# Kernel optimization log

Measured on AMD Instinct MI355X. Metric: run time of the kernel, lower is better.

The kernel has to match this reference:

```python
import jax, jax.numpy as jnp
import numpy as np

N = 10000   # num_nodes
P = 32      # input_dim
Q = 64      # output_dim
K = 2       # diffusion_steps
B = 32      # batch
E = 160000  # edges per transition matrix (avg degree 16)
M = 2 * K + 1  # num_matrices (dual random walk)


def setup_inputs() -> dict:
    key = jax.random.key(0)
    ks = jax.random.split(key, 8)
    inputs = jax.random.normal(ks[0], (B, N * P), dtype=jnp.float32)
    trans1_idx = jax.random.randint(ks[1], (2, E), 0, N, dtype=jnp.int32)
    trans1_val = jax.random.uniform(ks[2], (E,), dtype=jnp.float32)
    trans2_idx = jax.random.randint(ks[3], (2, E), 0, N, dtype=jnp.int32)
    trans2_val = jax.random.uniform(ks[4], (E,), dtype=jnp.float32)
    weight = jax.random.normal(ks[5], (P * M, Q), dtype=jnp.float32) * (1.414 / np.sqrt(P * M))
    bias = jnp.zeros((Q,), dtype=jnp.float32)
    return {"inputs": inputs, "trans1_idx": trans1_idx, "trans1_val": trans1_val,
            "trans2_idx": trans2_idx, "trans2_val": trans2_val,
            "weight": weight, "bias": bias}


def _spmm(idx, val, x):
    # sparse [N,N] (COO rows=idx[0], cols=idx[1]) @ dense x [N, F]
    gathered = val[:, None] * x[idx[1]]            # [E, F]
    return jax.ops.segment_sum(gathered, idx[0], num_segments=N)


def reference(inputs, trans1_idx, trans1_val, trans2_idx, trans2_val, weight, bias):
    batch_size = inputs.shape[0]
    # [B, N*P] -> [N, P*B] (matches torch transpose/reshape sequence)
    x0_base = inputs.reshape(batch_size, N, P).transpose(1, 2, 0).reshape(N, P * batch_size)
    xs = [x0_base]
    for idx, val in ((trans1_idx, trans1_val), (trans2_idx, trans2_val)):
        x0 = x0_base
        x1 = _spmm(idx, val, x0)
        xs.append(x1)
        for _ in range(2, K + 1):
            x2 = 2.0 * _spmm(idx, val, x1) - x0
            xs.append(x2)
            x1, x0 = x2, x1
    x = jnp.stack(xs)                                   # [M, N, P*B]
    x = x.reshape(M, N, P, batch_size).transpose(3, 1, 2, 0)  # [B, N, P, M]
    x = x.reshape(batch_size * N, P * M)
    out = x @ weight + bias                             # [B*N, Q]
    return out.reshape(batch_size, N * Q)
```

## Files before the change

kernel.cpp:

```cpp
#include <hip/hip_runtime.h>
#include <hip/hip_bf16.h>

#define NN 10000
#define PP 32
#define QQ 64
#define EE 160000
#define FF 1024
#define NQ 640000
#define SLOTS 64

typedef __attribute__((ext_vector_type(8))) short sh8;
typedef __attribute__((ext_vector_type(8))) __bf16 bf8v;
typedef __attribute__((ext_vector_type(4))) float f32x4;

__device__ __forceinline__ short f2bf(float f) {
    return __builtin_bit_cast(short, __float2bfloat16(f));
}

__global__ __launch_bounds__(256)
void pre_kernel(const float* __restrict__ in, short* __restrict__ x0,
                const float* __restrict__ W, short* __restrict__ wt,
                int* __restrict__ cnt, int2* __restrict__ ed1, int2* __restrict__ ed2) {
    int t = threadIdx.x;
    if (blockIdx.x == 0) {
#pragma unroll
        for (int j = 0; j < 40; ++j) {
            int idx = t + j * 256;
            int k = idx >> 6, q = idx & 63;
            int p = k / 5;
            int m = k - p * 5;
            wt[q * 160 + m * 32 + p] = f2bf(W[idx]);
        }
        return;
    }
    int n = blockIdx.x - 1;
    int b = t >> 3;
    int p0 = (t & 7) * 4;
    float4 v = *(const float4*)(in + (size_t)b * (NN * PP) + (size_t)n * PP + p0);
    short4 s = make_short4(f2bf(v.x), f2bf(v.y), f2bf(v.z), f2bf(v.w));
    *(short4*)(x0 + (size_t)n * FF + b * 32 + p0) = s;
    if (t < 32)      *(int4*)(ed1 + n * SLOTS + t * 2) = make_int4(0, 0, 0, 0);
    else if (t < 64) *(int4*)(ed2 + n * SLOTS + (t - 32) * 2) = make_int4(0, 0, 0, 0);
    else if (t == 64) { cnt[n] = 0; cnt[NN + n] = 0; }
}

__global__ __launch_bounds__(256)
void scatter_kernel(const int* __restrict__ t1i, const float* __restrict__ t1v,
                    const int* __restrict__ t2i, const float* __restrict__ t2v,
                    int* __restrict__ cnt, int2* __restrict__ ed1, int2* __restrict__ ed2) {
    int e = blockIdx.x * 256 + threadIdx.x;
    const int* idx; const float* val; int* cn; int2* ed; int ee;
    if (e < EE) { idx = t1i; val = t1v; cn = cnt;      ed = ed1; ee = e; }
    else        { idx = t2i; val = t2v; cn = cnt + NN; ed = ed2; ee = e - EE; }
    int r = idx[ee];
    int c = idx[EE + ee];
    int pos = atomicAdd(&cn[r], 1);
    if (pos < SLOTS) ed[r * SLOTS + pos] = make_int2(c, __float_as_int(val[ee]));
}

__global__ __launch_bounds__(256)
void spmm_kernel(const int* __restrict__ cnt, const int2* __restrict__ ed1,
                 const int2* __restrict__ ed2,
                 const short* __restrict__ x1s, const short* __restrict__ x2s,
                 short* __restrict__ out1, short* __restrict__ out2,
                 const short* __restrict__ sub, float alpha) {
    int bid = blockIdx.x;
    int c = bid & 7;
    int rest = bid >> 3;
    int rb = rest % 625;
    int g = rest / 625;
    int fbase = c * 128;
    int wid  = threadIdx.x >> 6;
    int lane = threadIdx.x & 63;
    int grp  = lane >> 4;
    int l8   = (lane & 15) * 8;
    int n = rb * 16 + wid * 4 + grp;

    const int2* ed; const __bf16* x; short* out; int cn;
    if (g == 0) { ed = ed1 + n * SLOTS; x = (const __bf16*)x1s; out = out1; cn = cnt[n]; }
    else        { ed = ed2 + n * SLOTS; x = (const __bf16*)x2s; out = out2; cn = cnt[NN + n]; }
    cn = min(cn, SLOTS);
    int iters = (cn + 3) >> 2;
    const __bf16* xp = x + fbase + l8;

    float acc[8];
#pragma unroll
    for (int j = 0; j < 8; ++j) acc[j] = 0.f;

    for (int it = 0; it < iters; ++it) {
        int4 dA = *(const int4*)(ed);
        int4 dB = *(const int4*)(ed + 2);
        ed += 4;
        bf8v xa = *(const bf8v*)(xp + ((size_t)(unsigned)dA.x << 10));
        bf8v xb = *(const bf8v*)(xp + ((size_t)(unsigned)dA.z << 10));
        bf8v xc = *(const bf8v*)(xp + ((size_t)(unsigned)dB.x << 10));
        bf8v xd = *(const bf8v*)(xp + ((size_t)(unsigned)dB.z << 10));
        float v0 = __int_as_float(dA.y), v1 = __int_as_float(dA.w);
        float v2 = __int_as_float(dB.y), v3 = __int_as_float(dB.w);
#pragma unroll
        for (int j = 0; j < 8; ++j) {
            acc[j] = fmaf((float)xa[j], v0, acc[j]);
            acc[j] = fmaf((float)xb[j], v1, acc[j]);
            acc[j] = fmaf((float)xc[j], v2, acc[j]);
            acc[j] = fmaf((float)xd[j], v3, acc[j]);
        }
    }

    size_t obase = (size_t)n * FF + fbase + l8;
    sh8 o;
    if (sub) {
        bf8v s = *(const bf8v*)((const __bf16*)sub + obase);
#pragma unroll
        for (int j = 0; j < 8; ++j) o[j] = f2bf(alpha * acc[j] - (float)s[j]);
    } else {
#pragma unroll
        for (int j = 0; j < 8; ++j) o[j] = f2bf(acc[j]);
    }
    *(sh8*)(out + obase) = o;
}

__global__ __launch_bounds__(256)
void gemm_mfma_kernel(const short* __restrict__ xs, const short* __restrict__ wt,
                      const float* __restrict__ bias, float* __restrict__ out) {
    int t = threadIdx.x;
    int lane = t & 63;
    int gw = blockIdx.x * 4 + (t >> 6);
    int c = lane & 15, hi = lane >> 4;

    sh8 a0[5], a1[5], a2[5], a3[5];
#pragma unroll
    for (int ks = 0; ks < 5; ++ks) {
        a0[ks] = *(const sh8*)(wt + (0 * 16 + c) * 160 + ks * 32 + hi * 8);
        a1[ks] = *(const sh8*)(wt + (1 * 16 + c) * 160 + ks * 32 + hi * 8);
        a2[ks] = *(const sh8*)(wt + (2 * 16 + c) * 160 + ks * 32 + hi * 8);
        a3[ks] = *(const sh8*)(wt + (3 * 16 + c) * 160 + ks * 32 + hi * 8);
    }
    float4 bv0 = *(const float4*)(bias + 0 * 16 + hi * 4);
    float4 bv1 = *(const float4*)(bias + 1 * 16 + hi * 4);
    float4 bv2 = *(const float4*)(bias + 2 * 16 + hi * 4);
    float4 bv3 = *(const float4*)(bias + 3 * 16 + hi * 4);

    for (int item = gw; item < 20000; item += 5000) {
        int b = item & 31, nt = item >> 5;
        const short* base = xs + (size_t)(nt * 16 + c) * FF + b * 32 + hi * 8;
        f32x4 acc0 = {0.f, 0.f, 0.f, 0.f};
        f32x4 acc1 = {0.f, 0.f, 0.f, 0.f};
        f32x4 acc2 = {0.f, 0.f, 0.f, 0.f};
        f32x4 acc3 = {0.f, 0.f, 0.f, 0.f};
#pragma unroll
        for (int ks = 0; ks < 5; ++ks) {
            sh8 bf = *(const sh8*)(base + (size_t)ks * ((size_t)NN * FF));
            acc0 = __builtin_amdgcn_mfma_f32_16x16x32_bf16(a0[ks], bf, acc0, 0, 0, 0);
            acc1 = __builtin_amdgcn_mfma_f32_16x16x32_bf16(a1[ks], bf, acc1, 0, 0, 0);
            acc2 = __builtin_amdgcn_mfma_f32_16x16x32_bf16(a2[ks], bf, acc2, 0, 0, 0);
            acc3 = __builtin_amdgcn_mfma_f32_16x16x32_bf16(a3[ks], bf, acc3, 0, 0, 0);
        }
        float* po = out + (size_t)b * NQ + (size_t)(nt * 16 + c) * 64 + hi * 4;
        *(float4*)(po +  0) = make_float4(acc0[0] + bv0.x, acc0[1] + bv0.y, acc0[2] + bv0.z, acc0[3] + bv0.w);
        *(float4*)(po + 16) = make_float4(acc1[0] + bv1.x, acc1[1] + bv1.y, acc1[2] + bv1.z, acc1[3] + bv1.w);
        *(float4*)(po + 32) = make_float4(acc2[0] + bv2.x, acc2[1] + bv2.y, acc2[2] + bv2.z, acc2[3] + bv2.w);
        *(float4*)(po + 48) = make_float4(acc3[0] + bv3.x, acc3[1] + bv3.y, acc3[2] + bv3.z, acc3[3] + bv3.w);
    }
}

extern "C" void kernel_launch(void* const* d_in, const int* in_sizes, int n_in,
                              void* d_out, int out_size, void* d_ws, size_t ws_size,
                              hipStream_t stream) {
    const float* inputs = (const float*)d_in[0];
    const int*   t1i    = (const int*)d_in[1];
    const float* t1v    = (const float*)d_in[2];
    const int*   t2i    = (const int*)d_in[3];
    const float* t2v    = (const float*)d_in[4];
    const float* W      = (const float*)d_in[5];
    const float* bias   = (const float*)d_in[6];
    float* out = (float*)d_out;

    short* ws = (short*)d_ws;
    const size_t NF = (size_t)NN * FF;
    short* x0  = ws;
    short* xs1 = ws + 1 * NF;
    short* xs2 = ws + 2 * NF;
    short* xs3 = ws + 3 * NF;
    short* xs4 = ws + 4 * NF;
    short* wt  = ws + 5 * NF;
    int* cnt  = (int*)(wt + 64 * 160);
    int2* ed1 = (int2*)(cnt + 2 * NN);
    int2* ed2 = ed1 + (size_t)NN * SLOTS;

    pre_kernel<<<NN + 1, 256, 0, stream>>>(inputs, x0, W, wt, cnt, ed1, ed2);
    scatter_kernel<<<(2 * EE) / 256, 256, 0, stream>>>(t1i, t1v, t2i, t2v, cnt, ed1, ed2);

    const int spmm_grid = 2 * 625 * 8;

    spmm_kernel<<<spmm_grid, 256, 0, stream>>>(cnt, ed1, ed2,
                                               x0, x0, xs1, xs3,
                                               nullptr, 1.0f);
    spmm_kernel<<<spmm_grid, 256, 0, stream>>>(cnt, ed1, ed2,
                                               xs1, xs3, xs2, xs4,
                                               x0, 2.0f);

    gemm_mfma_kernel<<<1250, 256, 0, stream>>>(ws, wt, bias, out);
}
```

Measured before the change: 167.4 us.

## Sort rows by degree for balanced SpMM waves and use packed bf16 math

Adds a counting-sort kernel that orders nodes by edge count, largest first, and has the SpMM kernels process rows in that permuted order. Rows with similar degree then share a wavefront, which cuts divergence and load imbalance. The scatter kernel now handles two edges per thread with vector loads. The SpMM inner loop converts bf16 with bit shifts and accumulates in packed float2 operations. The cost is an extra launch of a two-block sort kernel and one indirect perm lookup per row.

```diff
diff --git a/kernel.cpp b/kernel.cpp
--- a/kernel.cpp
+++ b/kernel.cpp
@@ -12,9 +12,17 @@
 typedef __attribute__((ext_vector_type(8))) short sh8;
 typedef __attribute__((ext_vector_type(8))) __bf16 bf8v;
 typedef __attribute__((ext_vector_type(4))) float f32x4;
+typedef __attribute__((ext_vector_type(2))) float f32x2;
 
 __device__ __forceinline__ short f2bf(float f) {
     return __builtin_bit_cast(short, __float2bfloat16(f));
+}
+
+__device__ __forceinline__ f32x2 cvt2(unsigned d) {
+    f32x2 r;
+    r.x = __uint_as_float(d << 16);
+    r.y = __uint_as_float(d & 0xffff0000u);
+    return r;
 }
 
 __global__ __launch_bounds__(256)
@@ -48,19 +56,48 @@
 void scatter_kernel(const int* __restrict__ t1i, const float* __restrict__ t1v,
                     const int* __restrict__ t2i, const float* __restrict__ t2v,
                     int* __restrict__ cnt, int2* __restrict__ ed1, int2* __restrict__ ed2) {
-    int e = blockIdx.x * 256 + threadIdx.x;
-    const int* idx; const float* val; int* cn; int2* ed; int ee;
-    if (e < EE) { idx = t1i; val = t1v; cn = cnt;      ed = ed1; ee = e; }
-    else        { idx = t2i; val = t2v; cn = cnt + NN; ed = ed2; ee = e - EE; }
-    int r = idx[ee];
-    int c = idx[EE + ee];
-    int pos = atomicAdd(&cn[r], 1);
-    if (pos < SLOTS) ed[r * SLOTS + pos] = make_int2(c, __float_as_int(val[ee]));
-}
-
-__global__ __launch_bounds__(256)
-void spmm_kernel(const int* __restrict__ cnt, const int2* __restrict__ ed1,
-                 const int2* __restrict__ ed2,
+    int tid = blockIdx.x * 256 + threadIdx.x;
+    const int* idx; const float* val; int* cn; int2* ed; int e0;
+    if (tid < EE / 2) { idx = t1i; val = t1v; cn = cnt;      ed = ed1; e0 = tid * 2; }
+    else              { idx = t2i; val = t2v; cn = cnt + NN; ed = ed2; e0 = (tid - EE / 2) * 2; }
+    int2 rr = *(const int2*)(idx + e0);
+    int2 cc = *(const int2*)(idx + EE + e0);
+    float2 vv = *(const float2*)(val + e0);
+    int pos0 = atomicAdd(&cn[rr.x], 1);
+    if (pos0 < SLOTS) ed[rr.x * SLOTS + pos0] = make_int2(cc.x, __float_as_int(vv.x));
+    int pos1 = atomicAdd(&cn[rr.y], 1);
+    if (pos1 < SLOTS) ed[rr.y * SLOTS + pos1] = make_int2(cc.y, __float_as_int(vv.y));
+}
+
+__global__ __launch_bounds__(1024)
+void sort_kernel(const int* __restrict__ cnt, int* __restrict__ perm) {
+    __shared__ int bins[65];
+    __shared__ int base[65];
+    int g = blockIdx.x;
+    const int* cn = cnt + g * NN;
+    int* pm = perm + g * NN;
+    int t = threadIdx.x;
+    if (t < 65) bins[t] = 0;
+    __syncthreads();
+    for (int i = t; i < NN; i += 1024) atomicAdd(&bins[min(cn[i], SLOTS)], 1);
+    __syncthreads();
+    if (t == 0) {
+        int run = 0;
+        for (int d = 64; d >= 0; --d) { base[d] = run; run += bins[d]; }
+    }
+    __syncthreads();
+    if (t < 65) bins[t] = base[t];
+    __syncthreads();
+    for (int i = t; i < NN; i += 1024) {
+        int d = min(cn[i], SLOTS);
+        int pos = atomicAdd(&bins[d], 1);
+        pm[pos] = i;
+    }
+}
+
+__global__ __launch_bounds__(256)
+void spmm_kernel(const int* __restrict__ cnt, const int* __restrict__ perm,
+                 const int2* __restrict__ ed1, const int2* __restrict__ ed2,
                  const short* __restrict__ x1s, const short* __restrict__ x2s,
                  short* __restrict__ out1, short* __restrict__ out2,
                  const short* __restrict__ sub, float alpha) {
@@ -74,7 +111,8 @@
     int lane = threadIdx.x & 63;
     int grp  = lane >> 4;
     int l8   = (lane & 15) * 8;
-    int n = rb * 16 + wid * 4 + grp;
+    int slot = rb * 16 + wid * 4 + grp;
+    int n = perm[g * NN + slot];
 
     const int2* ed; const __bf16* x; short* out; int cn;
     if (g == 0) { ed = ed1 + n * SLOTS; x = (const __bf16*)x1s; out = out1; cn = cnt[n]; }
@@ -83,38 +121,42 @@
     int iters = (cn + 3) >> 2;
     const __bf16* xp = x + fbase + l8;
 
-    float acc[8];
-#pragma unroll
-    for (int j = 0; j < 8; ++j) acc[j] = 0.f;
+    f32x2 acc0 = {0.f, 0.f}, acc1 = {0.f, 0.f}, acc2 = {0.f, 0.f}, acc3 = {0.f, 0.f};
 
     for (int it = 0; it < iters; ++it) {
         int4 dA = *(const int4*)(ed);
         int4 dB = *(const int4*)(ed + 2);
         ed += 4;
-        bf8v xa = *(const bf8v*)(xp + ((size_t)(unsigned)dA.x << 10));
-        bf8v xb = *(const bf8v*)(xp + ((size_t)(unsigned)dA.z << 10));
-        bf8v xc = *(const bf8v*)(xp + ((size_t)(unsigned)dB.x << 10));
-        bf8v xd = *(const bf8v*)(xp + ((size_t)(unsigned)dB.z << 10));
-        float v0 = __int_as_float(dA.y), v1 = __int_as_float(dA.w);
-        float v2 = __int_as_float(dB.y), v3 = __int_as_float(dB.w);
-#pragma unroll
-        for (int j = 0; j < 8; ++j) {
-            acc[j] = fmaf((float)xa[j], v0, acc[j]);
-            acc[j] = fmaf((float)xb[j], v1, acc[j]);
-            acc[j] = fmaf((float)xc[j], v2, acc[j]);
-            acc[j] = fmaf((float)xd[j], v3, acc[j]);
-        }
-    }
+        uint4 xa = *(const uint4*)(xp + ((unsigned)dA.x << 10));
+        uint4 xb = *(const uint4*)(xp + ((unsigned)dA.z << 10));
+        uint4 xc = *(const uint4*)(xp + ((unsigned)dB.x << 10));
+        uint4 xd = *(const uint4*)(xp + ((unsigned)dB.z << 10));
+        float s0 = __int_as_float(dA.y), s1 = __int_as_float(dA.w);
+        float s2 = __int_as_float(dB.y), s3 = __int_as_float(dB.w);
+        f32x2 v0 = {s0, s0}, v1 = {s1, s1}, v2 = {s2, s2}, v3 = {s3, s3};
+        acc0 += cvt2(xa.x) * v0; acc1 += cvt2(xa.y) * v0;
+        acc2 += cvt2(xa.z) * v0; acc3 += cvt2(xa.w) * v0;
+        acc0 += cvt2(xb.x) * v1; acc1 += cvt2(xb.y) * v1;
+        acc2 += cvt2(xb.z) * v1; acc3 += cvt2(xb.w) * v1;
+        acc0 += cvt2(xc.x) * v2; acc1 += cvt2(xc.y) * v2;
+        acc2 += cvt2(xc.z) * v2; acc3 += cvt2(xc.w) * v2;
+        acc0 += cvt2(xd.x) * v3; acc1 += cvt2(xd.y) * v3;
+        acc2 += cvt2(xd.z) * v3; acc3 += cvt2(xd.w) * v3;
+    }
+
+    float av[8];
+    av[0] = acc0.x; av[1] = acc0.y; av[2] = acc1.x; av[3] = acc1.y;
+    av[4] = acc2.x; av[5] = acc2.y; av[6] = acc3.x; av[7] = acc3.y;
 
     size_t obase = (size_t)n * FF + fbase + l8;
     sh8 o;
     if (sub) {
         bf8v s = *(const bf8v*)((const __bf16*)sub + obase);
 #pragma unroll
-        for (int j = 0; j < 8; ++j) o[j] = f2bf(alpha * acc[j] - (float)s[j]);
+        for (int j = 0; j < 8; ++j) o[j] = f2bf(alpha * av[j] - (float)s[j]);
     } else {
 #pragma unroll
-        for (int j = 0; j < 8; ++j) o[j] = f2bf(acc[j]);
+        for (int j = 0; j < 8; ++j) o[j] = f2bf(av[j]);
     }
     *(sh8*)(out + obase) = o;
 }
@@ -186,16 +228,18 @@
     int* cnt  = (int*)(wt + 64 * 160);
     int2* ed1 = (int2*)(cnt + 2 * NN);
     int2* ed2 = ed1 + (size_t)NN * SLOTS;
+    int* perm = (int*)(ed2 + (size_t)NN * SLOTS);
 
     pre_kernel<<<NN + 1, 256, 0, stream>>>(inputs, x0, W, wt, cnt, ed1, ed2);
-    scatter_kernel<<<(2 * EE) / 256, 256, 0, stream>>>(t1i, t1v, t2i, t2v, cnt, ed1, ed2);
+    scatter_kernel<<<EE / 256, 256, 0, stream>>>(t1i, t1v, t2i, t2v, cnt, ed1, ed2);
+    sort_kernel<<<2, 1024, 0, stream>>>(cnt, perm);
 
     const int spmm_grid = 2 * 625 * 8;
 
-    spmm_kernel<<<spmm_grid, 256, 0, stream>>>(cnt, ed1, ed2,
+    spmm_kernel<<<spmm_grid, 256, 0, stream>>>(cnt, perm, ed1, ed2,
                                                x0, x0, xs1, xs3,
                                                nullptr, 1.0f);
-    spmm_kernel<<<spmm_grid, 256, 0, stream>>>(cnt, ed1, ed2,
+    spmm_kernel<<<spmm_grid, 256, 0, stream>>>(cnt, perm, ed1, ed2,
                                                xs1, xs3, xs2, xs4,
                                                x0, 2.0f);
 
```

Result: no change. 164.6 us (-1.7%).
